# Optimization experiments

Measured on AMD Instinct MI355X. Metric: run time of the kernel, lower is better.

Reference implementation:

```python
import jax, jax.numpy as jnp
import numpy as np

EPS = 1e-5
GN_GROUPS = 4  # ConvBlock groupnorm num_groups

def _conv3d(x, w, b):
    # x: [B,C,D,H,W], w: [O,I,3,3,3]
    y = jax.lax.conv_general_dilated(x, w, (1, 1, 1), 'SAME',
                                     dimension_numbers=('NCDHW', 'OIDHW', 'NCDHW'))
    return y + b[None, :, None, None, None]

def _groupnorm(x, gamma, beta):
    b, c, d, h, w = x.shape
    xg = x.reshape(b, GN_GROUPS, c // GN_GROUPS, d, h, w)
    m = xg.mean(axis=(2, 3, 4, 5), keepdims=True)
    v = xg.var(axis=(2, 3, 4, 5), keepdims=True)
    xn = ((xg - m) * jax.lax.rsqrt(v + EPS)).reshape(b, c, d, h, w)
    return xn * gamma[None, :, None, None, None] + beta[None, :, None, None, None]

def setup_inputs() -> dict:
    key = jax.random.key(0)
    ks = jax.random.split(key, 8)
    B, C, D, H, W = 4, 64, 16, 16, 16
    R = 4
    f = lambda k, s: jax.random.normal(k, s, dtype=jnp.float32) * 0.05
    return {
        'x': jax.random.normal(ks[0], (B, C, D, H, W), dtype=jnp.float32),
        'w_i': f(ks[1], (C, C, 3, 3, 3)), 'b_i': jnp.zeros((C,), jnp.float32),
        'gamma_i': jnp.ones((C,), jnp.float32), 'beta_i': jnp.zeros((C,), jnp.float32),
        'w_q': f(ks[2], (C // R, C)), 'b_q': jnp.zeros((C // R,), jnp.float32),
        'w_k': f(ks[3], (C // R, C)), 'b_k': jnp.zeros((C // R,), jnp.float32),
        'w_v': f(ks[4], (C, C)), 'b_v': jnp.zeros((C,), jnp.float32),
        'w_o': f(ks[5], (C, C, 3, 3, 3)), 'b_o': jnp.zeros((C,), jnp.float32),
        'gamma_o': jnp.ones((C,), jnp.float32), 'beta_o': jnp.zeros((C,), jnp.float32),
    }

def reference(x, w_i, b_i, gamma_i, beta_i, w_q, b_q, w_k, b_k, w_v, b_v,
              w_o, b_o, gamma_o, beta_o):
    # i_conv: Conv3d(3x3x3) -> GroupNorm(4) -> ReLU
    x = jax.nn.relu(_groupnorm(_conv3d(x, w_i, b_i), gamma_i, beta_i))
    b, c, d, h, w = x.shape
    n = d * h * w
    xf = x.reshape(b, c, n)
    # spatial attention (groups=1): conv1x1 projections as channel matmuls
    q = jnp.einsum('oc,bcn->bon', w_q, xf) + b_q[None, :, None]   # [b, c/r, n]
    k = jnp.einsum('oc,bcn->bon', w_k, xf) + b_k[None, :, None]   # [b, c/r, n]
    v = jnp.einsum('oc,bcn->bon', w_v, xf) + b_v[None, :, None]   # [b, c,   n]
    A = jax.nn.softmax(jnp.einsum('bqn,bqm->bnm', q, k), axis=-1)  # [b, n, n]
    # ans = bmm(value, A^T): ans[b,c,m] = sum_n v[b,c,n] * A[b,m,n]
    sa = jnp.einsum('bcn,bmn->bcm', v, A).reshape(b, c, d, h, w)
    # channel attention
    Ac = jax.nn.softmax(jnp.einsum('bcn,bdn->bcd', xf, xf), axis=-1)  # [b, c, c]
    ca = jnp.einsum('bcd,bdn->bcn', Ac, xf).reshape(b, c, d, h, w)
    y = x + sa + ca
    # o_conv
    return jax.nn.relu(_groupnorm(_conv3d(y, w_o, b_o), gamma_o, beta_o))
```

## Files before the change

kernel.cpp:

```cpp
#include <hip/hip_runtime.h>

#define OFF_T0  0
#define OFF_SA  1048576
#define OFF_QT  2097152
#define OFF_KT  2359296
#define OFF_VB  2621440
#define OFF_YT  3145728
#define OFF_XB  3670016
#define OFF_AC  4194304
#define OFF_WBI 4210688
#define OFF_WBO 4265984
#define OFF_PT  4321280
#define OFF_PO  4325376
#define OFF_MS  6422528
#define WS_NEED ((size_t)6553600 * 4)

typedef __attribute__((ext_vector_type(8))) short short8v;
typedef __attribute__((ext_vector_type(4))) short short4v;
typedef __attribute__((ext_vector_type(4))) float f32x4;

__device__ __forceinline__ ushort f2bf(float f) {
  union { float f; unsigned u; } v; v.f = f;
  unsigned r = (v.u + 0x7fffu + ((v.u >> 16) & 1u)) >> 16;
  return (ushort)r;
}
__device__ __forceinline__ float bf2f(ushort u) {
  union { unsigned u; float f; } v; v.u = ((unsigned)u) << 16;
  return v.f;
}
__device__ __forceinline__ float max3f(float a, float b, float c) {
  return fmaxf(fmaxf(a, b), c);
}

__global__ __launch_bounds__(256) void cvt_k(const float* __restrict__ x, ushort* __restrict__ xb,
    float* __restrict__ pt, const float* __restrict__ wi, const float* __restrict__ wo,
    ushort* __restrict__ wbi, ushort* __restrict__ wbo, float* __restrict__ acr) {
  __shared__ ushort tl[64 * 72];
  int blk = blockIdx.x;
  int t = threadIdx.x;
  if (blk < 256) {
    int b = blk >> 6;
    int n0 = (blk & 63) * 64;
    int ci = t >> 2, q = t & 3;
    const float* src = x + (size_t)(b * 64 + ci) * 4096 + n0 + q * 16;
    #pragma unroll
    for (int i = 0; i < 4; ++i) {
      float4 v = *reinterpret_cast<const float4*>(src + i * 4);
      tl[(q * 16 + i * 4 + 0) * 72 + ci] = f2bf(v.x);
      tl[(q * 16 + i * 4 + 1) * 72 + ci] = f2bf(v.y);
      tl[(q * 16 + i * 4 + 2) * 72 + ci] = f2bf(v.z);
      tl[(q * 16 + i * 4 + 3) * 72 + ci] = f2bf(v.w);
    }
    __syncthreads();
    int n = t >> 2, qq = t & 3;
    ushort* dst = xb + (size_t)(b * 4096 + n0 + n) * 64 + qq * 16;
    *reinterpret_cast<short8v*>(dst) = *reinterpret_cast<const short8v*>(&tl[n * 72 + qq * 16]);
    *reinterpret_cast<short8v*>(dst + 8) = *reinterpret_cast<const short8v*>(&tl[n * 72 + qq * 16 + 8]);
  } else if (blk < 1120) {
    int idx = (blk - 256) * 256 + t;
    const float* w = idx < 110592 ? wi : wo;
    ushort* wb = idx < 110592 ? wbi : wbo;
    int j = idx < 110592 ? idx : idx - 110592;
    int ci = j & 63, tap = (j >> 6) % 27, co = j / (64 * 27);
    wb[j] = f2bf(w[(co * 64 + ci) * 27 + tap]);
  } else {
    int idx = (blk - 1120) * 256 + t;
    acr[idx] = 0.f;
    if (blk == 1120 && t < 64) pt[t] = 0.f;
  }
}

__global__ __launch_bounds__(256) void conv_mfma_k(const ushort* __restrict__ xt,
    const ushort* __restrict__ wb, const float* __restrict__ bias, float* __restrict__ out,
    float* __restrict__ ptg) {
  __shared__ __align__(16) ushort xls[18 * 18 * 64];
  __shared__ float sh_st[16];
  int blk = blockIdx.x;
  int h0 = (blk & 3) * 4;
  int d0 = (blk >> 2) & 15;
  int b  = blk >> 6;
  int tid = threadIdx.x;

  const ushort* xtb = xt + (size_t)b * 4096 * 64;
  for (int u = tid; u < 324; u += 256) {
    int w_s = u % 18;
    int row = u / 18;
    int dz = row / 6, h_s = row - dz * 6;
    int d = d0 + dz - 1, h = h0 + h_s - 1, w = w_s - 1;
    ushort* dst = &xls[(row * 18 + w_s) * 64];
    int swz = w_s & 7;
    if (d >= 0 && d < 16 && h >= 0 && h < 16 && w >= 0 && w < 16) {
      const ushort* src = xtb + (size_t)(d * 256 + h * 16 + w) * 64;
      #pragma unroll
      for (int c = 0; c < 8; ++c)
        *reinterpret_cast<short8v*>(dst + ((c ^ swz) << 3)) =
            *reinterpret_cast<const short8v*>(src + (c << 3));
    } else {
      short8v z = {};
      #pragma unroll
      for (int c = 0; c < 8; ++c)
        *reinterpret_cast<short8v*>(dst + ((c ^ swz) << 3)) = z;
    }
  }
  __syncthreads();

  int wv = tid >> 6, l = tid & 63;
  int wn = wv >> 1, wc = wv & 1;
  int lm = l & 15, lg = l >> 4;

  f32x4 acc[2][2] = {};
  const ushort* wbase0 = wb + (size_t)((wc * 2 + 0) * 16 + lm) * 1728 + lg * 8;
  const ushort* wbase1 = wb + (size_t)((wc * 2 + 1) * 16 + lm) * 1728 + lg * 8;

  #pragma unroll 6
  for (int s = 0; s < 54; ++s) {
    int tap = s >> 1, c0h = s & 1;
    int dz = tap / 9, dyx = tap - dz * 9;
    int dy = dyx / 3, dx = dyx - dy * 3;
    int wrow = lm + dx;
    int chunk = ((c0h * 4 + lg) ^ (wrow & 7)) << 3;
    int r0 = ((dz * 6 + wn * 2 + dy) * 18 + wrow) * 64 + chunk;
    short8v a0 = *reinterpret_cast<const short8v*>(&xls[r0]);
    short8v a1 = *reinterpret_cast<const short8v*>(&xls[r0 + 18 * 64]);
    short8v b0 = *reinterpret_cast<const short8v*>(wbase0 + s * 32);
    short8v b1 = *reinterpret_cast<const short8v*>(wbase1 + s * 32);
    acc[0][0] = __builtin_amdgcn_mfma_f32_16x16x32_bf16(a0, b0, acc[0][0], 0, 0, 0);
    acc[0][1] = __builtin_amdgcn_mfma_f32_16x16x32_bf16(a0, b1, acc[0][1], 0, 0, 0);
    acc[1][0] = __builtin_amdgcn_mfma_f32_16x16x32_bf16(a1, b0, acc[1][0], 0, 0, 0);
    acc[1][1] = __builtin_amdgcn_mfma_f32_16x16x32_bf16(a1, b1, acc[1][1], 0, 0, 0);
  }

  float gs[2], gss[2];
  #pragma unroll
  for (int j = 0; j < 2; ++j) {
    gs[j] = 0.f; gss[j] = 0.f;
    int co = (wc * 2 + j) * 16 + lm;
    float bs = bias[co];
    #pragma unroll
    for (int i = 0; i < 2; ++i) {
      int hh = h0 + wn * 2 + i;
      float4 o;
      o.x = acc[i][j][0] + bs; o.y = acc[i][j][1] + bs;
      o.z = acc[i][j][2] + bs; o.w = acc[i][j][3] + bs;
      gs[j]  += o.x + o.y + o.z + o.w;
      gss[j] = fmaf(o.x, o.x, gss[j]); gss[j] = fmaf(o.y, o.y, gss[j]);
      gss[j] = fmaf(o.z, o.z, gss[j]); gss[j] = fmaf(o.w, o.w, gss[j]);
      *reinterpret_cast<float4*>(&out[(size_t)(b * 64 + co) * 4096 + d0 * 256 + hh * 16 + lg * 4]) = o;
    }
  }
  #pragma unroll
  for (int j = 0; j < 2; ++j) {
    #pragma unroll
    for (int off = 32; off > 0; off >>= 1) {
      gs[j]  += __shfl_xor(gs[j], off);
      gss[j] += __shfl_xor(gss[j], off);
    }
    if (l == 0) { sh_st[wv * 4 + j * 2] = gs[j]; sh_st[wv * 4 + j * 2 + 1] = gss[j]; }
  }
  __syncthreads();
  if (tid < 8) {
    int g = tid >> 1, w2 = tid & 1;
    int wcg = g >> 1, j = g & 1;
    float v = sh_st[wcg * 4 + j * 2 + w2] + sh_st[(wcg + 2) * 4 + j * 2 + w2];
    atomicAdd(&ptg[(b * 4 + g) * 2 + w2], v);
  }
}

__global__ __launch_bounds__(256) void gn_apply_k(const float* __restrict__ t, const float* __restrict__ pt,
    const float* __restrict__ gamma, const float* __restrict__ beta, float* __restrict__ out) {
  int idx = blockIdx.x * 256 + threadIdx.x;
  int c = (idx >> 12) & 63, b = idx >> 18;
  int bg = b * 4 + (c >> 4);
  float s0 = pt[bg * 2], ss0 = pt[bg * 2 + 1];
  float m = s0 * (1.f / 65536.f);
  float r = rsqrtf(ss0 * (1.f / 65536.f) - m * m + 1e-5f);
  float ga = r * gamma[c], bb2 = beta[c] - m * r * gamma[c];
  out[idx] = fmaxf(fmaf(t[idx], ga, bb2), 0.f);
}

__global__ __launch_bounds__(256) void projgram_k(const float* __restrict__ t0, const float* __restrict__ pt0,
    const float* __restrict__ gamma, const float* __restrict__ beta,
    const float* __restrict__ wq, const float* __restrict__ bq,
    const float* __restrict__ wk, const float* __restrict__ bk,
    const float* __restrict__ wv_, const float* __restrict__ bv,
    ushort* __restrict__ qt, ushort* __restrict__ kt, ushort* __restrict__ vt,
    float* __restrict__ acr) {
  __shared__ __align__(16) float smem[64 * 68];
  int blk = blockIdx.x;
  int tid = threadIdx.x;
  if (blk < 256) {
    float* xls = smem;
    int b = blk >> 6, n0 = (blk & 63) * 64;
    {
      int ci = tid >> 2, q = tid & 3;
      int bg = b * 4 + (ci >> 4);
      float s0 = pt0[bg * 2], ss0 = pt0[bg * 2 + 1];
      float m = s0 * (1.f / 65536.f);
      float rv = rsqrtf(ss0 * (1.f / 65536.f) - m * m + 1e-5f);
      float ga = rv * gamma[ci], bb2 = beta[ci] - m * rv * gamma[ci];
      const float* src = t0 + (size_t)(b * 64 + ci) * 4096 + n0 + q * 16;
      #pragma unroll
      for (int i = 0; i < 4; ++i) {
        float4 v = *reinterpret_cast<const float4*>(src + i * 4);
        float* d = &xls[ci * 68 + q * 16 + i * 4];
        d[0] = fmaxf(fmaf(v.x, ga, bb2), 0.f);
        d[1] = fmaxf(fmaf(v.y, ga, bb2), 0.f);
        d[2] = fmaxf(fmaf(v.z, ga, bb2), 0.f);
        d[3] = fmaxf(fmaf(v.w, ga, bb2), 0.f);
      }
    }
    __syncthreads();
    int n = tid & 63, og = tid >> 6;
    float xr[64];
    #pragma unroll
    for (int c = 0; c < 64; ++c) xr[c] = xls[c * 68 + n];
    if (og < 2) {
      const float* w  = og == 0 ? wq : wk;
      const float* bb = og == 0 ? bq : bk;
      float scale = og == 0 ? 1.4426950408889634f : 1.0f;
      ushort* outp = og == 0 ? qt : kt;
      union { ushort u[16]; short8v v[2]; } pk;
      #pragma unroll
      for (int o = 0; o < 16; ++o) {
        const float* wr = w + o * 64;
        float acc = bb[o];
        #pragma unroll
        for (int c = 0; c < 64; ++c) acc = fmaf(wr[c], xr[c], acc);
        pk.u[o] = f2bf(acc * scale);
      }
      ushort* dst = outp + (size_t)(b * 4096 + n0 + n) * 32;
      *reinterpret_cast<short8v*>(dst) = pk.v[0];
      *reinterpret_cast<short8v*>(dst + 8) = pk.v[1];
      short8v z = {};
      *reinterpret_cast<short8v*>(dst + 16) = z;
      *reinterpret_cast<short8v*>(dst + 24) = z;
    } else {
      int o0 = (og - 2) * 32;
      #pragma unroll
      for (int o = 0; o < 32; ++o) {
        const float* wr = wv_ + (o0 + o) * 64;
        float acc = bv[o0 + o];
        #pragma unroll
        for (int c = 0; c < 64; ++c) acc = fmaf(wr[c], xr[c], acc);
        vt[(size_t)(b * 64 + o0 + o) * 4096 + n0 + n] = f2bf(acc);
      }
    }
  } else {
    ushort* hi = (ushort*)smem;
    ushort* lo = hi + 4096;
    int gblk = blk - 256;
    int b = gblk >> 5, ks = gblk & 31;
    int wv = tid >> 6, l = tid & 63, lm = l & 15, lg = l >> 4;
    int wr = wv >> 1, wd = wv & 1;
    f32x4 acc[2][2] = {};
    int sr = tid >> 2, sq = tid & 3;
    int bg = b * 4 + (sr >> 4);
    float s0p = pt0[bg * 2], ss0p = pt0[bg * 2 + 1];
    float mq = s0p * (1.f / 65536.f);
    float rq = rsqrtf(ss0p * (1.f / 65536.f) - mq * mq + 1e-5f);
    float ga = rq * gamma[sr], bb2 = beta[sr] - mq * rq * gamma[sr];
    const float* xb = t0 + (size_t)b * 262144;

    for (int kt2 = 0; kt2 < 2; ++kt2) {
      int n0 = ks * 128 + kt2 * 64;
      __syncthreads();
      const float* src = xb + (size_t)sr * 4096 + n0 + sq * 16;
      #pragma unroll
      for (int c2 = 0; c2 < 2; ++c2) {
        int chunk = sq * 2 + c2;
        int dchunk = chunk ^ (sr & 7);
        short8v hvv, lvv;
        #pragma unroll
        for (int j = 0; j < 8; ++j) {
          float v = fmaxf(fmaf(src[c2 * 8 + j], ga, bb2), 0.f);
          ushort hb = f2bf(v);
          union { float f; unsigned u; } uu; uu.u = ((unsigned)hb) << 16;
          hvv[j] = (short)hb;
          lvv[j] = (short)f2bf(v - uu.f);
        }
        *reinterpret_cast<short8v*>(hi + sr * 64 + dchunk * 8) = hvv;
        *reinterpret_cast<short8v*>(lo + sr * 64 + dchunk * 8) = lvv;
      }
      __syncthreads();
      #pragma unroll
      for (int kk = 0; kk < 2; ++kk) {
        short8v ah[2], al[2], bh[2], bl[2];
        #pragma unroll
        for (int i = 0; i < 2; ++i) {
          int rc = wr * 32 + i * 16 + lm;
          int ca = ((kk * 4 + lg) ^ (rc & 7)) * 8;
          ah[i] = *reinterpret_cast<const short8v*>(hi + rc * 64 + ca);
          al[i] = *reinterpret_cast<const short8v*>(lo + rc * 64 + ca);
          int rd = wd * 32 + i * 16 + lm;
          int cb = ((kk * 4 + lg) ^ (rd & 7)) * 8;
          bh[i] = *reinterpret_cast<const short8v*>(hi + rd * 64 + cb);
          bl[i] = *reinterpret_cast<const short8v*>(lo + rd * 64 + cb);
        }
        #pragma unroll
        for (int i = 0; i < 2; ++i)
          #pragma unroll
          for (int j = 0; j < 2; ++j) {
            acc[i][j] = __builtin_amdgcn_mfma_f32_16x16x32_bf16(ah[i], bh[j], acc[i][j], 0, 0, 0);
            acc[i][j] = __builtin_amdgcn_mfma_f32_16x16x32_bf16(ah[i], bl[j], acc[i][j], 0, 0, 0);
            acc[i][j] = __builtin_amdgcn_mfma_f32_16x16x32_bf16(al[i], bh[j], acc[i][j], 0, 0, 0);
          }
      }
    }
    float* acb = acr + (size_t)b * 4096;
    #pragma unroll
    for (int i = 0; i < 2; ++i)
      #pragma unroll
      for (int j = 0; j < 2; ++j)
        #pragma unroll
        for (int r = 0; r < 4; ++r) {
          int c = wr * 32 + i * 16 + lg * 4 + r;
          int d = wd * 32 + j * 16 + lm;
          atomicAdd(&acb[c * 64 + d], acc[i][j][r]);
        }
  }
}

#define KP 40
#define VP 72
template<bool SPLIT>
__global__ __launch_bounds__(256) void flash_mfma_k(const ushort* __restrict__ qt,
    const ushort* __restrict__ kt, const ushort* __restrict__ vb, float* __restrict__ sa,
    ushort* __restrict__ pacc, float* __restrict__ pms) {
  __shared__ __align__(16) ushort kls[2][64 * KP];
  __shared__ __align__(16) ushort vls[2][64 * VP];
  __shared__ __align__(16) ushort pls[64 * VP];
  int s, mt, b;
  if (SPLIT) { s = blockIdx.x & 3; mt = (blockIdx.x >> 2) & 63; b = blockIdx.x >> 8; }
  else       { s = 0; mt = blockIdx.x & 63; b = blockIdx.x >> 6; }
  const int NT = SPLIT ? 16 : 64;
  int m0 = mt * 64;
  int kofs = s * 1024;
  int tid = threadIdx.x;
  int w = tid >> 6, l = tid & 63;
  int lm = l & 15, lg = l >> 4;

  short8v qf = *reinterpret_cast<const short8v*>(
      qt + (size_t)(b * 4096 + m0 + w * 16 + lm) * 32 + lg * 8);

  f32x4 acc[4] = {};
  float M = -1e30f, S = 0.f;

  int sr = tid >> 2, sq = tid & 3;
  const ushort* ksrc = kt + (size_t)b * 4096 * 32 + (size_t)kofs * 32 + (size_t)sr * 32 + sq * 8;
  const ushort* vsrc = vb + (size_t)b * 64 * 4096 + (size_t)sr * 4096 + kofs + sq * 16;
  int koff = sr * KP + sq * 8;
  int voff = sr * VP + sq * 16;

  {
    short8v kr = *reinterpret_cast<const short8v*>(ksrc);
    short8v v0 = *reinterpret_cast<const short8v*>(vsrc);
    short8v v1 = *reinterpret_cast<const short8v*>(vsrc + 8);
    *reinterpret_cast<short8v*>(&kls[0][koff]) = kr;
    *reinterpret_cast<short8v*>(&vls[0][voff]) = v0;
    *reinterpret_cast<short8v*>(&vls[0][voff + 8]) = v1;
  }

  ushort* plb = &pls[(w * 16 + lm) * VP];

  #pragma unroll 2
  for (int it = 0; it < NT; ++it) {
    int cur = it & 1;
    int nx = it < NT - 1 ? it + 1 : NT - 1;
    short8v knr = *reinterpret_cast<const short8v*>(ksrc + (size_t)nx * 2048);
    short8v vn0 = *reinterpret_cast<const short8v*>(vsrc + nx * 64);
    short8v vn1 = *reinterpret_cast<const short8v*>(vsrc + nx * 64 + 8);

    __syncthreads();

    const ushort* kb  = &kls[cur][0];
    const ushort* vbk = &vls[cur][0];

    f32x4 sf[4];
    #pragma unroll
    for (int nt = 0; nt < 4; ++nt) {
      short8v kf = *reinterpret_cast<const short8v*>(&kb[(nt * 16 + lm) * KP + lg * 8]);
      f32x4 z = {};
      sf[nt] = __builtin_amdgcn_mfma_f32_16x16x32_bf16(kf, qf, z, 0, 0, 0);
    }

    float t0_ = max3f(sf[0][0], sf[0][1], sf[0][2]);
    float t1_ = max3f(sf[0][3], sf[1][0], sf[1][1]);
    float t2_ = max3f(sf[1][2], sf[1][3], sf[2][0]);
    float t3_ = max3f(sf[2][1], sf[2][2], sf[2][3]);
    float t4_ = max3f(sf[3][0], sf[3][1], sf[3][2]);
    float tmax = fmaxf(max3f(t0_, t1_, t2_), max3f(t3_, t4_, sf[3][3]));
    tmax = fmaxf(tmax, __shfl_xor(tmax, 16));
    tmax = fmaxf(tmax, __shfl_xor(tmax, 32));
    if (!__all(tmax <= M)) {
      float Mn = fmaxf(M, tmax);
      float sc = __builtin_amdgcn_exp2f(M - Mn);
      M = Mn;
      S *= sc;
      #pragma unroll
      for (int ct = 0; ct < 4; ++ct)
        #pragma unroll
        for (int r = 0; r < 4; ++r) acc[ct][r] *= sc;
    }
    float tsum = 0.f;
    float p[16];
    #pragma unroll
    for (int nt = 0; nt < 4; ++nt)
      #pragma unroll
      for (int r = 0; r < 4; ++r) {
        float e = __builtin_amdgcn_exp2f(sf[nt][r] - M);
        p[nt * 4 + r] = e;
        tsum += e;
      }
    tsum += __shfl_xor(tsum, 16);
    tsum += __shfl_xor(tsum, 32);
    S += tsum;

    #pragma unroll
    for (int nt = 0; nt < 4; ++nt) {
      unsigned p01, p23;
      asm("v_cvt_pk_bf16_f32 %0, %1, %2" : "=v"(p01) : "v"(p[nt * 4 + 0]), "v"(p[nt * 4 + 1]));
      asm("v_cvt_pk_bf16_f32 %0, %1, %2" : "=v"(p23) : "v"(p[nt * 4 + 2]), "v"(p[nt * 4 + 3]));
      union { unsigned u[2]; short4v v; } pk;
      pk.u[0] = p01; pk.u[1] = p23;
      *reinterpret_cast<short4v*>(plb + nt * 16 + lg * 4) = pk.v;
    }
    asm volatile("s_waitcnt lgkmcnt(0)" ::: "memory");
    __builtin_amdgcn_sched_barrier(0);

    #pragma unroll
    for (int nh = 0; nh < 2; ++nh) {
      short8v pf = *reinterpret_cast<const short8v*>(plb + nh * 32 + lg * 8);
      #pragma unroll
      for (int ct = 0; ct < 4; ++ct) {
        short8v vf = *reinterpret_cast<const short8v*>(&vbk[(ct * 16 + lm) * VP + nh * 32 + lg * 8]);
        acc[ct] = __builtin_amdgcn_mfma_f32_16x16x32_bf16(vf, pf, acc[ct], 0, 0, 0);
      }
    }

    if (it < NT - 1) {
      *reinterpret_cast<short8v*>(&kls[cur ^ 1][koff]) = knr;
      *reinterpret_cast<short8v*>(&vls[cur ^ 1][voff]) = vn0;
      *reinterpret_cast<short8v*>(&vls[cur ^ 1][voff + 8]) = vn1;
    }
  }

  if (SPLIT) {
    int blk2 = (b * 64 + mt) * 4 + s;
    ushort* pa = pacc + (size_t)blk2 * 4096;
    #pragma unroll
    for (int ct = 0; ct < 4; ++ct)
      #pragma unroll
      for (int r = 0; r < 4; ++r)
        pa[(ct * 16 + lg * 4 + r) * 64 + w * 16 + lm] = f2bf(acc[ct][r]);
    if (l < 16) {
      pms[(size_t)blk2 * 128 + (w * 16 + lm) * 2]     = M;
      pms[(size_t)blk2 * 128 + (w * 16 + lm) * 2 + 1] = S;
    }
  } else {
    float inv = 1.f / S;
    #pragma unroll
    for (int ct = 0; ct < 4; ++ct)
      #pragma unroll
      for (int r = 0; r < 4; ++r)
        sa[(size_t)(b * 64 + ct * 16 + lg * 4 + r) * 4096 + m0 + w * 16 + lm] = acc[ct][r] * inv;
  }
}

template<int NSPLIT>
__global__ __launch_bounds__(256) void ca_apply_k(const float* __restrict__ t0,
    const float* __restrict__ pt0, const float* __restrict__ gamma, const float* __restrict__ beta,
    const float* __restrict__ acr, const float* __restrict__ sa,
    const ushort* __restrict__ pacc, const float* __restrict__ pms, ushort* __restrict__ yt) {
  __shared__ float x1f[64 * 72];
  __shared__ float acf[64 * 72];
  __shared__ float wls[4 * 64];
  int b = blockIdx.x >> 6, mt = blockIdx.x & 63;
  int n0 = mt * 64;
  int tid = threadIdx.x;
  {
    int d = tid >> 2, q = tid & 3;
    int bg = b * 4 + (d >> 4);
    float s0p = pt0[bg * 2], ss0p = pt0[bg * 2 + 1];
    float mq = s0p * (1.f / 65536.f);
    float rq = rsqrtf(ss0p * (1.f / 65536.f) - mq * mq + 1e-5f);
    float ga = rq * gamma[d], bb2 = beta[d] - mq * rq * gamma[d];
    const float* xs = t0 + (size_t)(b * 64 + d) * 4096 + n0 + q * 16;
    const float* as = acr + (size_t)(b * 64 + d) * 64 + q * 16;
    #pragma unroll
    for (int i = 0; i < 4; ++i) {
      float4 v = *reinterpret_cast<const float4*>(xs + i * 4);
      x1f[d * 72 + q * 16 + i * 4 + 0] = fmaxf(fmaf(v.x, ga, bb2), 0.f);
      x1f[d * 72 + q * 16 + i * 4 + 1] = fmaxf(fmaf(v.y, ga, bb2), 0.f);
      x1f[d * 72 + q * 16 + i * 4 + 2] = fmaxf(fmaf(v.z, ga, bb2), 0.f);
      x1f[d * 72 + q * 16 + i * 4 + 3] = fmaxf(fmaf(v.w, ga, bb2), 0.f);
      float4 a = *reinterpret_cast<const float4*>(as + i * 4);
      acf[d * 72 + q * 16 + i * 4 + 0] = a.x;
      acf[d * 72 + q * 16 + i * 4 + 1] = a.y;
      acf[d * 72 + q * 16 + i * 4 + 2] = a.z;
      acf[d * 72 + q * 16 + i * 4 + 3] = a.w;
    }
  }
  if (NSPLIT > 1 && tid < 64) {
    int m = tid;
    size_t msb = (size_t)(b * 64 + mt) * NSPLIT * 128;
    float Ms[NSPLIT], Ss[NSPLIT];
    float Mg = -1e30f;
    #pragma unroll
    for (int s = 0; s < NSPLIT; ++s) {
      Ms[s] = pms[msb + s * 128 + m * 2];
      Ss[s] = pms[msb + s * 128 + m * 2 + 1];
      Mg = fmaxf(Mg, Ms[s]);
    }
    float Stot = 0.f;
    #pragma unroll
    for (int s = 0; s < NSPLIT; ++s) {
      float wv = __builtin_amdgcn_exp2f(Ms[s] - Mg);
      wls[s * 64 + m] = wv;
      Stot += wv * Ss[s];
    }
    float inv = 1.f / Stot;
    #pragma unroll
    for (int s = 0; s < NSPLIT; ++s) wls[s * 64 + m] *= inv;
  }
  __syncthreads();
  {
    int r = tid >> 2, q4 = tid & 3;
    float* row = &acf[r * 72 + q4 * 16];
    float mx = -1e30f;
    #pragma unroll
    for (int i = 0; i < 16; ++i) mx = fmaxf(mx, row[i]);
    mx = fmaxf(mx, __shfl_xor(mx, 1));
    mx = fmaxf(mx, __shfl_xor(mx, 2));
    float e[16];
    float sum = 0.f;
    #pragma unroll
    for (int i = 0; i < 16; ++i) { e[i] = __expf(row[i] - mx); sum += e[i]; }
    sum += __shfl_xor(sum, 1);
    sum += __shfl_xor(sum, 2);
    float inv = 1.f / sum;
    #pragma unroll
    for (int i = 0; i < 16; ++i) row[i] = e[i] * inv;
  }
  __syncthreads();
  int m = tid & 63, cg = tid >> 6;
  float sval[16];
  if (NSPLIT > 1) {
    #pragma unroll
    for (int ci = 0; ci < 16; ++ci) sval[ci] = 0.f;
    const ushort* pb = pacc + (size_t)(b * 64 + mt) * NSPLIT * 4096;
    #pragma unroll
    for (int s = 0; s < NSPLIT; ++s) {
      float wv = wls[s * 64 + m];
      #pragma unroll
      for (int ci = 0; ci < 16; ++ci)
        sval[ci] = fmaf(wv, bf2f(pb[s * 4096 + (cg * 16 + ci) * 64 + m]), sval[ci]);
    }
  } else {
    #pragma unroll
    for (int ci = 0; ci < 16; ++ci)
      sval[ci] = sa[(size_t)(b * 64 + cg * 16 + ci) * 4096 + n0 + m];
  }
  float xcol[64];
  #pragma unroll
  for (int d = 0; d < 64; ++d) xcol[d] = x1f[d * 72 + m];
  union { ushort u[16]; short8v v[2]; } pk;
  #pragma unroll
  for (int ci = 0; ci < 16; ++ci) {
    int c = cg * 16 + ci;
    float o = xcol[c] + sval[ci];
    const float* ar = &acf[c * 72];
    #pragma unroll
    for (int d4 = 0; d4 < 16; ++d4) {
      float4 a4 = *reinterpret_cast<const float4*>(ar + d4 * 4);
      o = fmaf(a4.x, xcol[d4 * 4 + 0], o);
      o = fmaf(a4.y, xcol[d4 * 4 + 1], o);
      o = fmaf(a4.z, xcol[d4 * 4 + 2], o);
      o = fmaf(a4.w, xcol[d4 * 4 + 3], o);
    }
    pk.u[ci] = f2bf(o);
  }
  ushort* dst = yt + (size_t)(b * 4096 + n0 + m) * 64 + cg * 16;
  *reinterpret_cast<short8v*>(dst) = pk.v[0];
  *reinterpret_cast<short8v*>(dst + 8) = pk.v[1];
}

extern "C" void kernel_launch(void* const* d_in, const int* in_sizes, int n_in,
                              void* d_out, int out_size, void* d_ws, size_t ws_size,
                              hipStream_t stream) {
  const float* x       = (const float*)d_in[0];
  const float* w_i     = (const float*)d_in[1];
  const float* b_i     = (const float*)d_in[2];
  const float* gamma_i = (const float*)d_in[3];
  const float* beta_i  = (const float*)d_in[4];
  const float* w_q     = (const float*)d_in[5];
  const float* b_q     = (const float*)d_in[6];
  const float* w_k     = (const float*)d_in[7];
  const float* b_k     = (const float*)d_in[8];
  const float* w_v     = (const float*)d_in[9];
  const float* b_v     = (const float*)d_in[10];
  const float* w_o     = (const float*)d_in[11];
  const float* b_o     = (const float*)d_in[12];
  const float* gamma_o = (const float*)d_in[13];
  const float* beta_o  = (const float*)d_in[14];
  float* ws = (float*)d_ws;
  float* t0 = ws + OFF_T0;
  ushort* qt  = (ushort*)(ws + OFF_QT);
  ushort* kt  = (ushort*)(ws + OFF_KT);
  ushort* vbp = (ushort*)(ws + OFF_VB);
  float* yb = ws + OFF_SA;
  ushort* ytp = (ushort*)(ws + OFF_YT);
  ushort* xbp = (ushort*)(ws + OFF_XB);
  float* acr = ws + OFF_AC;
  ushort* wbi = (ushort*)(ws + OFF_WBI);
  ushort* wbo = (ushort*)(ws + OFF_WBO);
  float* pt0 = ws + OFF_PT;
  float* pt1 = pt0 + 32;
  ushort* pacc = (ushort*)(ws + OFF_PO);
  float* pms  = ws + OFF_MS;
  float* outp = (float*)d_out;
  bool split = ws_size >= WS_NEED;

  cvt_k<<<1184, 256, 0, stream>>>(x, xbp, pt0, w_i, w_o, wbi, wbo, acr);

  conv_mfma_k<<<256, 256, 0, stream>>>(xbp, wbi, b_i, t0, pt0);

  projgram_k<<<384, 256, 0, stream>>>(t0, pt0, gamma_i, beta_i,
                                      w_q, b_q, w_k, b_k, w_v, b_v, qt, kt, vbp, acr);

  if (split)
    flash_mfma_k<true><<<1024, 256, 0, stream>>>(qt, kt, vbp, yb, pacc, pms);
  else
    flash_mfma_k<false><<<256, 256, 0, stream>>>(qt, kt, vbp, yb, pacc, pms);

  if (split)
    ca_apply_k<4><<<256, 256, 0, stream>>>(t0, pt0, gamma_i, beta_i, acr, yb, pacc, pms, ytp);
  else
    ca_apply_k<1><<<256, 256, 0, stream>>>(t0, pt0, gamma_i, beta_i, acr, yb, pacc, pms, ytp);

  conv_mfma_k<<<256, 256, 0, stream>>>(ytp, wbo, b_o, t0, pt1);
  gn_apply_k<<<4096, 256, 0, stream>>>(t0, pt1, gamma_o, beta_o, outp);
}
```

Baseline: 119.7 us.

## Fuse GroupNorm+ReLU into conv kernel via grid-wide barrier

The conv kernel now keeps its bias-added accumulators in registers, publishes group statistics, and waits on a global atomic counter until all 256 blocks have contributed. It then applies GroupNorm and ReLU directly and writes normalized output. This removes the separate gn_apply kernel and the re-normalization in projgram and ca_apply, which saves a full-tensor read/write pass and a launch. The cost is a spin-wait barrier that assumes all 256 blocks are co-resident on the device.

```diff
diff --git a/kernel.cpp b/kernel.cpp
--- a/kernel.cpp
+++ b/kernel.cpp
@@ -1,6 +1,6 @@
 #include <hip/hip_runtime.h>
 
-#define OFF_T0  0
+#define OFF_X1  0
 #define OFF_SA  1048576
 #define OFF_QT  2097152
 #define OFF_KT  2359296
@@ -66,13 +66,14 @@
   } else {
     int idx = (blk - 1120) * 256 + t;
     acr[idx] = 0.f;
-    if (blk == 1120 && t < 64) pt[t] = 0.f;
+    if (blk == 1120 && t < 128) pt[t] = 0.f;
   }
 }
 
 __global__ __launch_bounds__(256) void conv_mfma_k(const ushort* __restrict__ xt,
-    const ushort* __restrict__ wb, const float* __restrict__ bias, float* __restrict__ out,
-    float* __restrict__ ptg) {
+    const ushort* __restrict__ wb, const float* __restrict__ bias,
+    const float* __restrict__ gamma, const float* __restrict__ beta,
+    float* __restrict__ ptg, unsigned* __restrict__ cnt, float* __restrict__ out) {
   __shared__ __align__(16) ushort xls[18 * 18 * 64];
   __shared__ float sh_st[16];
   int blk = blockIdx.x;
@@ -137,16 +138,14 @@
     int co = (wc * 2 + j) * 16 + lm;
     float bs = bias[co];
     #pragma unroll
-    for (int i = 0; i < 2; ++i) {
-      int hh = h0 + wn * 2 + i;
-      float4 o;
-      o.x = acc[i][j][0] + bs; o.y = acc[i][j][1] + bs;
-      o.z = acc[i][j][2] + bs; o.w = acc[i][j][3] + bs;
-      gs[j]  += o.x + o.y + o.z + o.w;
-      gss[j] = fmaf(o.x, o.x, gss[j]); gss[j] = fmaf(o.y, o.y, gss[j]);
-      gss[j] = fmaf(o.z, o.z, gss[j]); gss[j] = fmaf(o.w, o.w, gss[j]);
-      *reinterpret_cast<float4*>(&out[(size_t)(b * 64 + co) * 4096 + d0 * 256 + hh * 16 + lg * 4]) = o;
-    }
+    for (int i = 0; i < 2; ++i)
+      #pragma unroll
+      for (int r = 0; r < 4; ++r) {
+        float o = acc[i][j][r] + bs;
+        acc[i][j][r] = o;
+        gs[j] += o;
+        gss[j] = fmaf(o, o, gss[j]);
+      }
   }
   #pragma unroll
   for (int j = 0; j < 2; ++j) {
@@ -164,22 +163,38 @@
     float v = sh_st[wcg * 4 + j * 2 + w2] + sh_st[(wcg + 2) * 4 + j * 2 + w2];
     atomicAdd(&ptg[(b * 4 + g) * 2 + w2], v);
   }
-}
-
-__global__ __launch_bounds__(256) void gn_apply_k(const float* __restrict__ t, const float* __restrict__ pt,
-    const float* __restrict__ gamma, const float* __restrict__ beta, float* __restrict__ out) {
-  int idx = blockIdx.x * 256 + threadIdx.x;
-  int c = (idx >> 12) & 63, b = idx >> 18;
-  int bg = b * 4 + (c >> 4);
-  float s0 = pt[bg * 2], ss0 = pt[bg * 2 + 1];
-  float m = s0 * (1.f / 65536.f);
-  float r = rsqrtf(ss0 * (1.f / 65536.f) - m * m + 1e-5f);
-  float ga = r * gamma[c], bb2 = beta[c] - m * r * gamma[c];
-  out[idx] = fmaxf(fmaf(t[idx], ga, bb2), 0.f);
-}
-
-__global__ __launch_bounds__(256) void projgram_k(const float* __restrict__ t0, const float* __restrict__ pt0,
-    const float* __restrict__ gamma, const float* __restrict__ beta,
+  __syncthreads();
+  if (tid == 0) {
+    __threadfence();
+    __hip_atomic_fetch_add(cnt, 1u, __ATOMIC_ACQ_REL, __HIP_MEMORY_SCOPE_AGENT);
+    while (__hip_atomic_load(cnt, __ATOMIC_ACQUIRE, __HIP_MEMORY_SCOPE_AGENT) < 256u) {
+      __builtin_amdgcn_s_sleep(2);
+    }
+  }
+  __syncthreads();
+  #pragma unroll
+  for (int j = 0; j < 2; ++j) {
+    int g = wc * 2 + j;
+    float s0  = __hip_atomic_load(&ptg[(b * 4 + g) * 2],     __ATOMIC_RELAXED, __HIP_MEMORY_SCOPE_AGENT);
+    float ss0 = __hip_atomic_load(&ptg[(b * 4 + g) * 2 + 1], __ATOMIC_RELAXED, __HIP_MEMORY_SCOPE_AGENT);
+    float m = s0 * (1.f / 65536.f);
+    float rv = rsqrtf(ss0 * (1.f / 65536.f) - m * m + 1e-5f);
+    int co = g * 16 + lm;
+    float ga = rv * gamma[co], bb2 = beta[co] - m * rv * gamma[co];
+    #pragma unroll
+    for (int i = 0; i < 2; ++i) {
+      int hh = h0 + wn * 2 + i;
+      float4 o;
+      o.x = fmaxf(fmaf(acc[i][j][0], ga, bb2), 0.f);
+      o.y = fmaxf(fmaf(acc[i][j][1], ga, bb2), 0.f);
+      o.z = fmaxf(fmaf(acc[i][j][2], ga, bb2), 0.f);
+      o.w = fmaxf(fmaf(acc[i][j][3], ga, bb2), 0.f);
+      *reinterpret_cast<float4*>(&out[(size_t)(b * 64 + co) * 4096 + d0 * 256 + hh * 16 + lg * 4]) = o;
+    }
+  }
+}
+
+__global__ __launch_bounds__(256) void projgram_k(const float* __restrict__ x1,
     const float* __restrict__ wq, const float* __restrict__ bq,
     const float* __restrict__ wk, const float* __restrict__ bk,
     const float* __restrict__ wv_, const float* __restrict__ bv,
@@ -193,20 +208,12 @@
     int b = blk >> 6, n0 = (blk & 63) * 64;
     {
       int ci = tid >> 2, q = tid & 3;
-      int bg = b * 4 + (ci >> 4);
-      float s0 = pt0[bg * 2], ss0 = pt0[bg * 2 + 1];
-      float m = s0 * (1.f / 65536.f);
-      float rv = rsqrtf(ss0 * (1.f / 65536.f) - m * m + 1e-5f);
-      float ga = rv * gamma[ci], bb2 = beta[ci] - m * rv * gamma[ci];
-      const float* src = t0 + (size_t)(b * 64 + ci) * 4096 + n0 + q * 16;
+      const float* src = x1 + (size_t)(b * 64 + ci) * 4096 + n0 + q * 16;
       #pragma unroll
       for (int i = 0; i < 4; ++i) {
         float4 v = *reinterpret_cast<const float4*>(src + i * 4);
         float* d = &xls[ci * 68 + q * 16 + i * 4];
-        d[0] = fmaxf(fmaf(v.x, ga, bb2), 0.f);
-        d[1] = fmaxf(fmaf(v.y, ga, bb2), 0.f);
-        d[2] = fmaxf(fmaf(v.z, ga, bb2), 0.f);
-        d[3] = fmaxf(fmaf(v.w, ga, bb2), 0.f);
+        d[0] = v.x; d[1] = v.y; d[2] = v.z; d[3] = v.w;
       }
     }
     __syncthreads();
@@ -254,12 +261,7 @@
     int wr = wv >> 1, wd = wv & 1;
     f32x4 acc[2][2] = {};
     int sr = tid >> 2, sq = tid & 3;
-    int bg = b * 4 + (sr >> 4);
-    float s0p = pt0[bg * 2], ss0p = pt0[bg * 2 + 1];
-    float mq = s0p * (1.f / 65536.f);
-    float rq = rsqrtf(ss0p * (1.f / 65536.f) - mq * mq + 1e-5f);
-    float ga = rq * gamma[sr], bb2 = beta[sr] - mq * rq * gamma[sr];
-    const float* xb = t0 + (size_t)b * 262144;
+    const float* xb = x1 + (size_t)b * 262144;
 
     for (int kt2 = 0; kt2 < 2; ++kt2) {
       int n0 = ks * 128 + kt2 * 64;
@@ -272,7 +274,7 @@
         short8v hvv, lvv;
         #pragma unroll
         for (int j = 0; j < 8; ++j) {
-          float v = fmaxf(fmaf(src[c2 * 8 + j], ga, bb2), 0.f);
+          float v = src[c2 * 8 + j];
           ushort hb = f2bf(v);
           union { float f; unsigned u; } uu; uu.u = ((unsigned)hb) << 16;
           hvv[j] = (short)hb;
@@ -467,8 +469,7 @@
 }
 
 template<int NSPLIT>
-__global__ __launch_bounds__(256) void ca_apply_k(const float* __restrict__ t0,
-    const float* __restrict__ pt0, const float* __restrict__ gamma, const float* __restrict__ beta,
+__global__ __launch_bounds__(256) void ca_apply_k(const float* __restrict__ x1,
     const float* __restrict__ acr, const float* __restrict__ sa,
     const ushort* __restrict__ pacc, const float* __restrict__ pms, ushort* __restrict__ yt) {
   __shared__ float x1f[64 * 72];
@@ -479,20 +480,15 @@
   int tid = threadIdx.x;
   {
     int d = tid >> 2, q = tid & 3;
-    int bg = b * 4 + (d >> 4);
-    float s0p = pt0[bg * 2], ss0p = pt0[bg * 2 + 1];
-    float mq = s0p * (1.f / 65536.f);
-    float rq = rsqrtf(ss0p * (1.f / 65536.f) - mq * mq + 1e-5f);
-    float ga = rq * gamma[d], bb2 = beta[d] - mq * rq * gamma[d];
-    const float* xs = t0 + (size_t)(b * 64 + d) * 4096 + n0 + q * 16;
+    const float* xs = x1 + (size_t)(b * 64 + d) * 4096 + n0 + q * 16;
     const float* as = acr + (size_t)(b * 64 + d) * 64 + q * 16;
     #pragma unroll
     for (int i = 0; i < 4; ++i) {
       float4 v = *reinterpret_cast<const float4*>(xs + i * 4);
-      x1f[d * 72 + q * 16 + i * 4 + 0] = fmaxf(fmaf(v.x, ga, bb2), 0.f);
-      x1f[d * 72 + q * 16 + i * 4 + 1] = fmaxf(fmaf(v.y, ga, bb2), 0.f);
-      x1f[d * 72 + q * 16 + i * 4 + 2] = fmaxf(fmaf(v.z, ga, bb2), 0.f);
-      x1f[d * 72 + q * 16 + i * 4 + 3] = fmaxf(fmaf(v.w, ga, bb2), 0.f);
+      x1f[d * 72 + q * 16 + i * 4 + 0] = v.x;
+      x1f[d * 72 + q * 16 + i * 4 + 1] = v.y;
+      x1f[d * 72 + q * 16 + i * 4 + 2] = v.z;
+      x1f[d * 72 + q * 16 + i * 4 + 3] = v.w;
       float4 a = *reinterpret_cast<const float4*>(as + i * 4);
       acf[d * 72 + q * 16 + i * 4 + 0] = a.x;
       acf[d * 72 + q * 16 + i * 4 + 1] = a.y;
@@ -603,7 +599,7 @@
   const float* gamma_o = (const float*)d_in[13];
   const float* beta_o  = (const float*)d_in[14];
   float* ws = (float*)d_ws;
-  float* t0 = ws + OFF_T0;
+  float* x1 = ws + OFF_X1;
   ushort* qt  = (ushort*)(ws + OFF_QT);
   ushort* kt  = (ushort*)(ws + OFF_KT);
   ushort* vbp = (ushort*)(ws + OFF_VB);
@@ -615,6 +611,8 @@
   ushort* wbo = (ushort*)(ws + OFF_WBO);
   float* pt0 = ws + OFF_PT;
   float* pt1 = pt0 + 32;
+  unsigned* cnt0 = (unsigned*)(pt0 + 64);
+  unsigned* cnt1 = (unsigned*)(pt0 + 65);
   ushort* pacc = (ushort*)(ws + OFF_PO);
   float* pms  = ws + OFF_MS;
   float* outp = (float*)d_out;
@@ -622,10 +620,9 @@
 
   cvt_k<<<1184, 256, 0, stream>>>(x, xbp, pt0, w_i, w_o, wbi, wbo, acr);
 
-  conv_mfma_k<<<256, 256, 0, stream>>>(xbp, wbi, b_i, t0, pt0);
-
-  projgram_k<<<384, 256, 0, stream>>>(t0, pt0, gamma_i, beta_i,
-                                      w_q, b_q, w_k, b_k, w_v, b_v, qt, kt, vbp, acr);
+  conv_mfma_k<<<256, 256, 0, stream>>>(xbp, wbi, b_i, gamma_i, beta_i, pt0, cnt0, x1);
+
+  projgram_k<<<384, 256, 0, stream>>>(x1, w_q, b_q, w_k, b_k, w_v, b_v, qt, kt, vbp, acr);
 
   if (split)
     flash_mfma_k<true><<<1024, 256, 0, stream>>>(qt, kt, vbp, yb, pacc, pms);
@@ -633,10 +630,9 @@
     flash_mfma_k<false><<<256, 256, 0, stream>>>(qt, kt, vbp, yb, pacc, pms);
 
   if (split)
-    ca_apply_k<4><<<256, 256, 0, stream>>>(t0, pt0, gamma_i, beta_i, acr, yb, pacc, pms, ytp);
+    ca_apply_k<4><<<256, 256, 0, stream>>>(x1, acr, yb, pacc, pms, ytp);
   else
-    ca_apply_k<1><<<256, 256, 0, stream>>>(t0, pt0, gamma_i, beta_i, acr, yb, pacc, pms, ytp);
-
-  conv_mfma_k<<<256, 256, 0, stream>>>(ytp, wbo, b_o, t0, pt1);
-  gn_apply_k<<<4096, 256, 0, stream>>>(t0, pt1, gamma_o, beta_o, outp);
-}
+    ca_apply_k<1><<<256, 256, 0, stream>>>(x1, acr, yb, pacc, pms, ytp);
+
+  conv_mfma_k<<<256, 256, 0, stream>>>(ytp, wbo, b_o, gamma_o, beta_o, pt1, cnt1, outp);
+}
```

After: 143.7 us. 1.2x slower.
